# Kernel tuning notes

Hardware: AMD Instinct MI355X
Metric: run time of the kernel (lower is better)

Reference implementation:

```python
import jax, jax.numpy as jnp
import numpy as np

FFT_LENGTH = 2048
HOP_LENGTH = 512  # window_length // 4, window_length == fft_length


def _hann_periodic(n):
    # tf.signal.hann_window(n, periodic=True)
    return (0.5 - 0.5 * jnp.cos(2.0 * jnp.pi * jnp.arange(n) / n)).astype(jnp.float32)


def setup_inputs() -> dict:
    key = jax.random.key(0)
    k1, k2 = jax.random.split(key)
    B, F, NB = 4, 4000, FFT_LENGTH // 2 + 1
    spec_real = jax.random.normal(k1, (B, F, NB), dtype=jnp.float32)
    spec_imag = jax.random.normal(k2, (B, F, NB), dtype=jnp.float32)
    return {"spec_real": spec_real, "spec_imag": spec_imag}


def reference(spec_real, spec_imag) -> jnp.ndarray:
    fft_length, hop = FFT_LENGTH, HOP_LENGTH
    B, F, _ = spec_real.shape
    window = _hann_periodic(fft_length)  # [N], window_length == fft_length so no padding

    # irfft of the complex spectrogram -> time-domain frames [B, F, N]
    frames = jnp.fft.irfft(spec_real + 1j * spec_imag, n=fft_length).astype(jnp.float32)
    windowed = window * frames  # [B, F, N]

    # overlap-and-add: output length L = (F-1)*hop + N
    L = (F - 1) * hop + fft_length
    idx = (jnp.arange(F) * hop)[:, None] + jnp.arange(fft_length)[None, :]  # [F, N]
    out = jnp.zeros((B, L), jnp.float32).at[:, idx].add(windowed)

    # librosa window_sumsquare: overlap-add of squared window, guard tiny values
    wsq = jnp.zeros((L,), jnp.float32).at[idx].add(window * window)
    tiny = jnp.float32(np.finfo(np.float32).tiny)
    window_sum = jnp.where(wsq > tiny, wsq, jnp.float32(1.0))

    y = out / window_sum
    # center=True: trim fft_length//2 on each side
    half = fft_length // 2
    return y[:, half:L - half]
```

## Files before the change

kernel.cpp:

```cpp
#include <hip/hip_runtime.h>
#include <math.h>

#define NB       1025
#define M        1024
#define FFTN     2048
#define HOP      512
#define NFRAMES  4000
#define BATCH    4
#define OUT_T    2047488
#define R_HOPS   8
#define NPAIR    251
#define NWG      (BATCH * NPAIR)
#define PI_F     3.14159265358979323846f

__device__ __forceinline__ float2 cmul(float2 a, float2 b) {
    return make_float2(a.x*b.x - a.y*b.y, a.x*b.y + a.y*b.x);
}
__device__ __forceinline__ float4 cmul4(float4 v, float2 w) {
    return make_float4(v.x*w.x - v.y*w.y, v.x*w.y + v.y*w.x,
                       v.z*w.x - v.w*w.y, v.z*w.y + v.w*w.x);
}
__device__ __forceinline__ float4 f4add(float4 a, float4 b){ return make_float4(a.x+b.x, a.y+b.y, a.z+b.z, a.w+b.w); }
__device__ __forceinline__ float4 f4sub(float4 a, float4 b){ return make_float4(a.x-b.x, a.y-b.y, a.z-b.z, a.w-b.w); }
__device__ __forceinline__ float4 f4addi(float4 a, float4 b){ return make_float4(a.x-b.y, a.y+b.x, a.z-b.w, a.w+b.z); }
__device__ __forceinline__ float4 f4subi(float4 a, float4 b){ return make_float4(a.x+b.y, a.y-b.x, a.z+b.w, a.w-b.z); }

__device__ __forceinline__ int SW4(int i) { return i ^ ((i >> 3) & 7); }

__device__ __forceinline__ float wsq_at(int p) {
    int u  = p + FFTN / 2;
    int fm = u >> 9;
    int n0 = u & 511;
    float wsq = 0.f;
    #pragma unroll
    for (int jj = 0; jj < 4; ++jj) {
        int fr = fm - jj;
        if (fr >= 0 && fr < NFRAMES) {
            int n = n0 + (jj << 9);
            float sw = __sinf((PI_F / (float)FFTN) * (float)n);
            float w  = sw * sw;
            wsq += w * w;
        }
    }
    const float tiny = 1.17549435e-38f;
    return (wsq > tiny) ? wsq : 1.0f;
}
__device__ __forceinline__ float invw_at(int p, bool edge) {
    if (edge && (p < 512 || p >= OUT_T - 512)) return 1.0f / wsq_at(p);
    return (2.0f / 3.0f);
}

template<int ST>
__device__ __forceinline__ void stage4x(const float4* __restrict__ src,
                                        float4* __restrict__ dst, int j, float2 w1) {
    const int Ns = 1 << (2 * ST);
    float4 v0 = src[SW4(j)];
    float4 v1 = src[SW4(j + 256)];
    float4 v2 = src[SW4(j + 512)];
    float4 v3 = src[SW4(j + 768)];
    float2 w2 = cmul(w1, w1);
    float2 w3 = cmul(w2, w1);
    v1 = cmul4(v1, w1); v2 = cmul4(v2, w2); v3 = cmul4(v3, w3);
    float4 t0 = f4add(v0, v2), t1 = f4sub(v0, v2);
    float4 t2 = f4add(v1, v3), t3 = f4sub(v1, v3);
    int jm = j & (Ns - 1);
    int idxD = ((j >> (2 * ST)) << (2 * ST + 2)) + jm;
    dst[SW4(idxD         )] = f4add(t0, t2);
    dst[SW4(idxD +     Ns)] = f4addi(t1, t3);
    dst[SW4(idxD + 2 * Ns)] = f4sub(t0, t2);
    dst[SW4(idxD + 3 * Ns)] = f4subi(t1, t3);
}

__device__ __forceinline__ void load_spec(const float* __restrict__ sr,
                                          const float* __restrict__ si,
                                          int b, int f, int j,
                                          float* car, float* cai,
                                          float* cbr, float* cbi) {
    const size_t fb = ((size_t)b * NFRAMES + f) * NB;
    const float* __restrict__ xr = sr + fb;
    const float* __restrict__ xi = si + fb;
    #pragma unroll
    for (int kk = 0; kk < 4; ++kk) {
        int k  = j + kk * 256;
        int mk = M - k;
        car[kk] = xr[k];  cai[kk] = xi[k];
        cbr[kk] = xr[mk]; cbi[kk] = xi[mk];
    }
}

__device__ __forceinline__ void pack2_st0(float4* __restrict__ dst, int j,
                                          const float2* twp,
                                          const float* a1r, const float* a1i,
                                          const float* b1r, const float* b1i,
                                          const float* a2r, const float* a2i,
                                          const float* b2r, const float* b2i) {
    float4 z[4];
    #pragma unroll
    for (int kk = 0; kk < 4; ++kk) {
        float ar = a1r[kk], ai = a1i[kk], br = b1r[kk], bi = b1i[kk];
        float cr = a2r[kk], ci = a2i[kk], dr = b2r[kk], di = b2i[kk];
        if (kk == 0 && j == 0) { ai = 0.f; bi = 0.f; ci = 0.f; di = 0.f; }
        float2 t = twp[kk];
        float Er = 0.5f*(ar+br), Ei = 0.5f*(ai-bi), Dr = 0.5f*(ar-br), Di = 0.5f*(ai+bi);
        float Or = Dr*t.x - Di*t.y, Oi = Dr*t.y + Di*t.x;
        float Fr = 0.5f*(cr+dr), Fi = 0.5f*(ci-di), Gr = 0.5f*(cr-dr), Gi = 0.5f*(ci+di);
        float Pr = Gr*t.x - Gi*t.y, Pi = Gr*t.y + Gi*t.x;
        z[kk] = make_float4(Er - Oi, Ei + Or, Fr - Pi, Fi + Pr);
    }
    float4 t0 = f4add(z[0], z[2]), t1 = f4sub(z[0], z[2]);
    float4 t2 = f4add(z[1], z[3]), t3 = f4sub(z[1], z[3]);
    dst[SW4(4*j    )] = f4add(t0, t2);
    dst[SW4(4*j + 1)] = f4addi(t1, t3);
    dst[SW4(4*j + 2)] = f4sub(t0, t2);
    dst[SW4(4*j + 3)] = f4subi(t1, t3);
}

__global__ __launch_bounds__(256) void istft_pair_kernel(
    const float* __restrict__ sr, const float* __restrict__ si,
    float* __restrict__ out)
{
    __shared__ float4 buf0[M];
    __shared__ float4 buf1[M];

    int blk;
    {
        const int o   = blockIdx.x;
        const int xcd = o & 7, k = o >> 3;
        const int q = NWG / 8, r = NWG % 8;
        blk = (xcd < r ? xcd * (q + 1) : r * (q + 1) + (xcd - r) * q) + k;
    }

    const int b    = blk / NPAIR;
    const int pr   = blk - b * NPAIR;
    const int regA = 2 * pr;
    const int s0hA = regA * R_HOPS;
    const int s0hB = s0hA + R_HOPS;
    const int j    = threadIdx.x;
    const bool edgeA = (regA == 0) || (regA == 500);
    const bool edgeB = (regA + 1 == 500);

    float2 tw_pack[4];
    #pragma unroll
    for (int kk = 0; kk < 4; ++kk) {
        int k = j + kk * 256;
        float s, c;
        __sincosf(PI_F * (float)k * (1.0f / (float)M), &s, &c);
        tw_pack[kk] = make_float2(c, s);
    }
    float2 w1s[4];
    #pragma unroll
    for (int st = 1; st <= 4; ++st) {
        int Ns = 1 << (2 * st);
        int jm = j & (Ns - 1);
        float ang = (0.5f * PI_F / (float)Ns) * (float)jm;
        float s1, c1;
        __sincosf(ang, &s1, &c1);
        w1s[st-1] = make_float2(c1, s1);
    }
    float wreg[4][2];
    #pragma unroll
    for (int q = 0; q < 4; ++q) {
        int n = j + q * 256;
        #pragma unroll
        for (int h = 0; h < 2; ++h) {
            int t = 2 * n + h;
            float swv = __sinf((PI_F / (float)FFTN) * (float)t);
            wreg[q][h] = swv * swv * (1.0f / 1024.0f);
        }
    }

    float2 AccA[R_HOPS], AccB[R_HOPS];
    #pragma unroll
    for (int s = 0; s < R_HOPS; ++s) {
        AccA[s] = make_float2(0.f, 0.f);
        AccB[s] = make_float2(0.f, 0.f);
    }

    #pragma unroll
    for (int it = 0; it < 11; ++it) {
        const int fA = s0hA - 3 + it;
        const int fB = s0hB - 3 + it;
        const bool vA = (fA >= 0) && (fA < NFRAMES);
        const bool vB = (fB >= 0) && (fB < NFRAMES);
        if (!vA && !vB) continue;

        int fAc = fA < 0 ? 0 : (fA > NFRAMES-1 ? NFRAMES-1 : fA);
        int fBc = fB < 0 ? 0 : (fB > NFRAMES-1 ? NFRAMES-1 : fB);

        float a1r[4], a1i[4], b1r[4], b1i[4];
        float a2r[4], a2i[4], b2r[4], b2i[4];
        load_spec(sr, si, b, fAc, j, a1r, a1i, b1r, b1i);
        load_spec(sr, si, b, fBc, j, a2r, a2i, b2r, b2i);

        pack2_st0(buf0, j, tw_pack, a1r, a1i, b1r, b1i, a2r, a2i, b2r, b2i);
        __syncthreads();
        stage4x<1>(buf0, buf1, j, w1s[0]);
        __syncthreads();
        stage4x<2>(buf1, buf0, j, w1s[1]);
        __syncthreads();
        stage4x<3>(buf0, buf1, j, w1s[2]);
        __syncthreads();

        {
            float4 v0 = buf1[SW4(j)];
            float4 v1 = buf1[SW4(j + 256)];
            float4 v2 = buf1[SW4(j + 512)];
            float4 v3 = buf1[SW4(j + 768)];
            float2 w1 = w1s[3];
            float2 w2 = cmul(w1, w1);
            float2 w3 = cmul(w2, w1);
            v1 = cmul4(v1, w1); v2 = cmul4(v2, w2); v3 = cmul4(v3, w3);
            float4 t0 = f4add(v0, v2), t1 = f4sub(v0, v2);
            float4 t2 = f4add(v1, v3), t3 = f4sub(v1, v3);
            float4 g[4];
            g[0] = f4add(t0, t2);
            g[1] = f4addi(t1, t3);
            g[2] = f4sub(t0, t2);
            g[3] = f4subi(t1, t3);
            if (vA) {
                #pragma unroll
                for (int q = 0; q < 4; ++q) {
                    const int s = it - 3 + q;
                    if (s >= 0 && s < R_HOPS) {
                        AccA[s].x += g[q].x * wreg[q][0];
                        AccA[s].y += g[q].y * wreg[q][1];
                    }
                }
            }
            if (vB) {
                #pragma unroll
                for (int q = 0; q < 4; ++q) {
                    const int s = it - 3 + q;
                    if (s >= 0 && s < R_HOPS) {
                        AccB[s].x += g[q].z * wreg[q][0];
                        AccB[s].y += g[q].w * wreg[q][1];
                    }
                }
            }
        }
    }

    float* outb = out + (size_t)b * OUT_T;
    {
        const int base_u = s0hA * HOP;
        #pragma unroll
        for (int s = 0; s < R_HOPS; ++s) {
            int i2 = j + 256 * s;
            int p0 = base_u + 2 * i2 - FFTN / 2;
            int p1 = p0 + 1;
            if ((unsigned)p0 < (unsigned)OUT_T) outb[p0] = AccA[s].x * invw_at(p0, edgeA);
            if ((unsigned)p1 < (unsigned)OUT_T) outb[p1] = AccA[s].y * invw_at(p1, edgeA);
        }
    }
    {
        const int base_u = s0hB * HOP;
        #pragma unroll
        for (int s = 0; s < R_HOPS; ++s) {
            int i2 = j + 256 * s;
            int p0 = base_u + 2 * i2 - FFTN / 2;
            int p1 = p0 + 1;
            if ((unsigned)p0 < (unsigned)OUT_T) outb[p0] = AccB[s].x * invw_at(p0, edgeB);
            if ((unsigned)p1 < (unsigned)OUT_T) outb[p1] = AccB[s].y * invw_at(p1, edgeB);
        }
    }
}

extern "C" void kernel_launch(void* const* d_in, const int* in_sizes, int n_in,
                              void* d_out, int out_size, void* d_ws, size_t ws_size,
                              hipStream_t stream) {
    const float* sr = (const float*)d_in[0];
    const float* si = (const float*)d_in[1];
    float* out = (float*)d_out;
    istft_pair_kernel<<<NWG, 256, 0, stream>>>(sr, si, out);
}
```

Baseline: 53.49 us.

## Split FFT into per-wave sub-FFTs with wave-local sync and prefetch next frame

```diff
diff --git a/kernel.cpp b/kernel.cpp
--- a/kernel.cpp
+++ b/kernel.cpp
@@ -13,6 +13,12 @@
 #define NWG      (BATCH * NPAIR)
 #define PI_F     3.14159265358979323846f
 
+#define WAVE_WAIT()                                            \
+    do {                                                       \
+        asm volatile("s_waitcnt lgkmcnt(0)" ::: "memory");     \
+        __builtin_amdgcn_sched_barrier(0);                     \
+    } while (0)
+
 __device__ __forceinline__ float2 cmul(float2 a, float2 b) {
     return make_float2(a.x*b.x - a.y*b.y, a.x*b.y + a.y*b.x);
 }
@@ -51,76 +57,32 @@
 }
 
 template<int ST>
-__device__ __forceinline__ void stage4x(const float4* __restrict__ src,
-                                        float4* __restrict__ dst, int j, float2 w1) {
+__device__ __forceinline__ void stage256(const float4* __restrict__ src,
+                                         float4* __restrict__ dst, int l, float2 w1) {
     const int Ns = 1 << (2 * ST);
-    float4 v0 = src[SW4(j)];
-    float4 v1 = src[SW4(j + 256)];
-    float4 v2 = src[SW4(j + 512)];
-    float4 v3 = src[SW4(j + 768)];
+    float4 v0 = src[SW4(l)];
+    float4 v1 = src[SW4(l + 64)];
+    float4 v2 = src[SW4(l + 128)];
+    float4 v3 = src[SW4(l + 192)];
     float2 w2 = cmul(w1, w1);
     float2 w3 = cmul(w2, w1);
     v1 = cmul4(v1, w1); v2 = cmul4(v2, w2); v3 = cmul4(v3, w3);
     float4 t0 = f4add(v0, v2), t1 = f4sub(v0, v2);
     float4 t2 = f4add(v1, v3), t3 = f4sub(v1, v3);
-    int jm = j & (Ns - 1);
-    int idxD = ((j >> (2 * ST)) << (2 * ST + 2)) + jm;
+    int jm = l & (Ns - 1);
+    int idxD = ((l >> (2 * ST)) << (2 * ST + 2)) + jm;
     dst[SW4(idxD         )] = f4add(t0, t2);
     dst[SW4(idxD +     Ns)] = f4addi(t1, t3);
     dst[SW4(idxD + 2 * Ns)] = f4sub(t0, t2);
     dst[SW4(idxD + 3 * Ns)] = f4subi(t1, t3);
 }
 
-__device__ __forceinline__ void load_spec(const float* __restrict__ sr,
-                                          const float* __restrict__ si,
-                                          int b, int f, int j,
-                                          float* car, float* cai,
-                                          float* cbr, float* cbi) {
-    const size_t fb = ((size_t)b * NFRAMES + f) * NB;
-    const float* __restrict__ xr = sr + fb;
-    const float* __restrict__ xi = si + fb;
-    #pragma unroll
-    for (int kk = 0; kk < 4; ++kk) {
-        int k  = j + kk * 256;
-        int mk = M - k;
-        car[kk] = xr[k];  cai[kk] = xi[k];
-        cbr[kk] = xr[mk]; cbi[kk] = xi[mk];
-    }
-}
-
-__device__ __forceinline__ void pack2_st0(float4* __restrict__ dst, int j,
-                                          const float2* twp,
-                                          const float* a1r, const float* a1i,
-                                          const float* b1r, const float* b1i,
-                                          const float* a2r, const float* a2i,
-                                          const float* b2r, const float* b2i) {
-    float4 z[4];
-    #pragma unroll
-    for (int kk = 0; kk < 4; ++kk) {
-        float ar = a1r[kk], ai = a1i[kk], br = b1r[kk], bi = b1i[kk];
-        float cr = a2r[kk], ci = a2i[kk], dr = b2r[kk], di = b2i[kk];
-        if (kk == 0 && j == 0) { ai = 0.f; bi = 0.f; ci = 0.f; di = 0.f; }
-        float2 t = twp[kk];
-        float Er = 0.5f*(ar+br), Ei = 0.5f*(ai-bi), Dr = 0.5f*(ar-br), Di = 0.5f*(ai+bi);
-        float Or = Dr*t.x - Di*t.y, Oi = Dr*t.y + Di*t.x;
-        float Fr = 0.5f*(cr+dr), Fi = 0.5f*(ci-di), Gr = 0.5f*(cr-dr), Gi = 0.5f*(ci+di);
-        float Pr = Gr*t.x - Gi*t.y, Pi = Gr*t.y + Gi*t.x;
-        z[kk] = make_float4(Er - Oi, Ei + Or, Fr - Pi, Fi + Pr);
-    }
-    float4 t0 = f4add(z[0], z[2]), t1 = f4sub(z[0], z[2]);
-    float4 t2 = f4add(z[1], z[3]), t3 = f4sub(z[1], z[3]);
-    dst[SW4(4*j    )] = f4add(t0, t2);
-    dst[SW4(4*j + 1)] = f4addi(t1, t3);
-    dst[SW4(4*j + 2)] = f4sub(t0, t2);
-    dst[SW4(4*j + 3)] = f4subi(t1, t3);
-}
-
-__global__ __launch_bounds__(256) void istft_pair_kernel(
+__global__ __launch_bounds__(256) void istft_ws_kernel(
     const float* __restrict__ sr, const float* __restrict__ si,
     float* __restrict__ out)
 {
-    __shared__ float4 buf0[M];
-    __shared__ float4 buf1[M];
+    __shared__ float4 bufA[M];
+    __shared__ float4 bufB[M];
 
     int blk;
     {
@@ -135,32 +97,44 @@
     const int regA = 2 * pr;
     const int s0hA = regA * R_HOPS;
     const int s0hB = s0hA + R_HOPS;
-    const int j    = threadIdx.x;
+    const int tid  = threadIdx.x;
+    const int l    = tid & 63;
+    const int wv   = tid >> 6;
     const bool edgeA = (regA == 0) || (regA == 500);
     const bool edgeB = (regA + 1 == 500);
 
+    float4* __restrict__ wA = bufA + wv * 256;
+    float4* __restrict__ wB = bufB + wv * 256;
+
     float2 tw_pack[4];
     #pragma unroll
-    for (int kk = 0; kk < 4; ++kk) {
-        int k = j + kk * 256;
+    for (int e = 0; e < 4; ++e) {
+        int k = 4 * (l + 64 * e) + wv;
         float s, c;
-        __sincosf(PI_F * (float)k * (1.0f / (float)M), &s, &c);
-        tw_pack[kk] = make_float2(c, s);
-    }
-    float2 w1s[4];
-    #pragma unroll
-    for (int st = 1; st <= 4; ++st) {
+        __sincosf(PI_F * (float)k * (1.0f / 1024.0f), &s, &c);
+        tw_pack[e] = make_float2(c, s);
+    }
+    float2 w1s[3];
+    #pragma unroll
+    for (int st = 1; st <= 3; ++st) {
         int Ns = 1 << (2 * st);
-        int jm = j & (Ns - 1);
+        int jm = l & (Ns - 1);
         float ang = (0.5f * PI_F / (float)Ns) * (float)jm;
         float s1, c1;
         __sincosf(ang, &s1, &c1);
         w1s[st-1] = make_float2(c1, s1);
     }
+    float2 wg1, wg2, wg3;
+    {
+        float s, c;
+        __sincosf((PI_F / 512.f) * (float)tid, &s, &c);        wg1 = make_float2(c, s);
+        __sincosf((PI_F / 512.f) * (float)(2 * tid), &s, &c);  wg2 = make_float2(c, s);
+        __sincosf((PI_F / 512.f) * (float)(3 * tid), &s, &c);  wg3 = make_float2(c, s);
+    }
     float wreg[4][2];
     #pragma unroll
     for (int q = 0; q < 4; ++q) {
-        int n = j + q * 256;
+        int n = tid + q * 256;
         #pragma unroll
         for (int h = 0; h < 2; ++h) {
             int t = 2 * n + h;
@@ -174,6 +148,24 @@
     for (int s = 0; s < R_HOPS; ++s) {
         AccA[s] = make_float2(0.f, 0.f);
         AccB[s] = make_float2(0.f, 0.f);
+    }
+
+    float a1r[4], a1i[4], b1r[4], b1i[4];
+    float a2r[4], a2i[4], b2r[4], b2i[4];
+    {
+        int fA0 = s0hA - 3; fA0 = fA0 < 0 ? 0 : (fA0 > NFRAMES-1 ? NFRAMES-1 : fA0);
+        int fB0 = s0hB - 3; fB0 = fB0 < 0 ? 0 : (fB0 > NFRAMES-1 ? NFRAMES-1 : fB0);
+        const size_t fbA = ((size_t)b * NFRAMES + fA0) * NB;
+        const size_t fbB = ((size_t)b * NFRAMES + fB0) * NB;
+        #pragma unroll
+        for (int e = 0; e < 4; ++e) {
+            int k  = 4 * (l + 64 * e) + wv;
+            int mk = 1024 - k;
+            a1r[e] = sr[fbA + k];  a1i[e] = si[fbA + k];
+            b1r[e] = sr[fbA + mk]; b1i[e] = si[fbA + mk];
+            a2r[e] = sr[fbB + k];  a2i[e] = si[fbB + k];
+            b2r[e] = sr[fbB + mk]; b2i[e] = si[fbB + mk];
+        }
     }
 
     #pragma unroll
@@ -184,34 +176,61 @@
         const bool vB = (fB >= 0) && (fB < NFRAMES);
         if (!vA && !vB) continue;
 
-        int fAc = fA < 0 ? 0 : (fA > NFRAMES-1 ? NFRAMES-1 : fA);
-        int fBc = fB < 0 ? 0 : (fB > NFRAMES-1 ? NFRAMES-1 : fB);
-
-        float a1r[4], a1i[4], b1r[4], b1i[4];
-        float a2r[4], a2i[4], b2r[4], b2i[4];
-        load_spec(sr, si, b, fAc, j, a1r, a1i, b1r, b1i);
-        load_spec(sr, si, b, fBc, j, a2r, a2i, b2r, b2i);
-
-        pack2_st0(buf0, j, tw_pack, a1r, a1i, b1r, b1i, a2r, a2i, b2r, b2i);
+        {
+            float4 z[4];
+            #pragma unroll
+            for (int e = 0; e < 4; ++e) {
+                int k = 4 * (l + 64 * e) + wv;
+                float ar = a1r[e], ai = a1i[e], br = b1r[e], bi = b1i[e];
+                float cr = a2r[e], ci = a2i[e], dr = b2r[e], di = b2i[e];
+                if (k == 0) { ai = 0.f; bi = 0.f; ci = 0.f; di = 0.f; }
+                float2 t = tw_pack[e];
+                float Er = 0.5f*(ar+br), Ei = 0.5f*(ai-bi), Dr = 0.5f*(ar-br), Di = 0.5f*(ai+bi);
+                float Or = Dr*t.x - Di*t.y, Oi = Dr*t.y + Di*t.x;
+                float Fr = 0.5f*(cr+dr), Fi = 0.5f*(ci-di), Gr = 0.5f*(cr-dr), Gi = 0.5f*(ci+di);
+                float Pr = Gr*t.x - Gi*t.y, Pi = Gr*t.y + Gi*t.x;
+                z[e] = make_float4(Er - Oi, Ei + Or, Fr - Pi, Fi + Pr);
+            }
+            float4 t0 = f4add(z[0], z[2]), t1 = f4sub(z[0], z[2]);
+            float4 t2 = f4add(z[1], z[3]), t3 = f4sub(z[1], z[3]);
+            wA[SW4(4*l    )] = f4add(t0, t2);
+            wA[SW4(4*l + 1)] = f4addi(t1, t3);
+            wA[SW4(4*l + 2)] = f4sub(t0, t2);
+            wA[SW4(4*l + 3)] = f4subi(t1, t3);
+        }
+
+        if (it < 10) {
+            int fAn = fA + 1; fAn = fAn < 0 ? 0 : (fAn > NFRAMES-1 ? NFRAMES-1 : fAn);
+            int fBn = fB + 1; fBn = fBn < 0 ? 0 : (fBn > NFRAMES-1 ? NFRAMES-1 : fBn);
+            const size_t fbA = ((size_t)b * NFRAMES + fAn) * NB;
+            const size_t fbB = ((size_t)b * NFRAMES + fBn) * NB;
+            #pragma unroll
+            for (int e = 0; e < 4; ++e) {
+                int k  = 4 * (l + 64 * e) + wv;
+                int mk = 1024 - k;
+                a1r[e] = sr[fbA + k];  a1i[e] = si[fbA + k];
+                b1r[e] = sr[fbA + mk]; b1i[e] = si[fbA + mk];
+                a2r[e] = sr[fbB + k];  a2i[e] = si[fbB + k];
+                b2r[e] = sr[fbB + mk]; b2i[e] = si[fbB + mk];
+            }
+        }
+
+        WAVE_WAIT();
+        stage256<1>(wA, wB, l, w1s[0]);
+        WAVE_WAIT();
+        stage256<2>(wB, wA, l, w1s[1]);
+        WAVE_WAIT();
+        stage256<3>(wA, wB, l, w1s[2]);
+
         __syncthreads();
-        stage4x<1>(buf0, buf1, j, w1s[0]);
-        __syncthreads();
-        stage4x<2>(buf1, buf0, j, w1s[1]);
-        __syncthreads();
-        stage4x<3>(buf0, buf1, j, w1s[2]);
-        __syncthreads();
 
         {
-            float4 v0 = buf1[SW4(j)];
-            float4 v1 = buf1[SW4(j + 256)];
-            float4 v2 = buf1[SW4(j + 512)];
-            float4 v3 = buf1[SW4(j + 768)];
-            float2 w1 = w1s[3];
-            float2 w2 = cmul(w1, w1);
-            float2 w3 = cmul(w2, w1);
-            v1 = cmul4(v1, w1); v2 = cmul4(v2, w2); v3 = cmul4(v3, w3);
-            float4 t0 = f4add(v0, v2), t1 = f4sub(v0, v2);
-            float4 t2 = f4add(v1, v3), t3 = f4sub(v1, v3);
+            float4 T0 = bufB[        SW4(tid)];
+            float4 T1 = cmul4(bufB[256 + SW4(tid)], wg1);
+            float4 T2 = cmul4(bufB[512 + SW4(tid)], wg2);
+            float4 T3 = cmul4(bufB[768 + SW4(tid)], wg3);
+            float4 t0 = f4add(T0, T2), t1 = f4sub(T0, T2);
+            float4 t2 = f4add(T1, T3), t3 = f4sub(T1, T3);
             float4 g[4];
             g[0] = f4add(t0, t2);
             g[1] = f4addi(t1, t3);
@@ -238,6 +257,7 @@
                 }
             }
         }
+        __syncthreads();
     }
 
     float* outb = out + (size_t)b * OUT_T;
@@ -245,7 +265,7 @@
         const int base_u = s0hA * HOP;
         #pragma unroll
         for (int s = 0; s < R_HOPS; ++s) {
-            int i2 = j + 256 * s;
+            int i2 = tid + 256 * s;
             int p0 = base_u + 2 * i2 - FFTN / 2;
             int p1 = p0 + 1;
             if ((unsigned)p0 < (unsigned)OUT_T) outb[p0] = AccA[s].x * invw_at(p0, edgeA);
@@ -256,7 +276,7 @@
         const int base_u = s0hB * HOP;
         #pragma unroll
         for (int s = 0; s < R_HOPS; ++s) {
-            int i2 = j + 256 * s;
+            int i2 = tid + 256 * s;
             int p0 = base_u + 2 * i2 - FFTN / 2;
             int p1 = p0 + 1;
             if ((unsigned)p0 < (unsigned)OUT_T) outb[p0] = AccB[s].x * invw_at(p0, edgeB);
@@ -271,5 +291,5 @@
     const float* sr = (const float*)d_in[0];
     const float* si = (const float*)d_in[1];
     float* out = (float*)d_out;
-    istft_pair_kernel<<<NWG, 256, 0, stream>>>(sr, si, out);
-}
+    istft_ws_kernel<<<NWG, 256, 0, stream>>>(sr, si, out);
+}
```

Result: slower. 99.75 us (+86.5%).
